# Kernel optimization log

Measured on AMD Instinct MI355X. Metric: run time of the kernel, lower is better.

Reference implementation:

```python
import jax, jax.numpy as jnp
import numpy as np

N_SRC = 50000
N_DST = 50000
N_EDGES = 500000
HIDDEN = 128
HEADS = 8
HEAD_DIM = HIDDEN // HEADS
SCALE = HEAD_DIM ** -0.5


def setup_inputs() -> dict:
    key = jax.random.key(0)
    ks = jax.random.split(key, 12)
    lim = 1.0 / np.sqrt(HIDDEN)
    def lin(k):
        kw, kb = jax.random.split(k)
        W = jax.random.uniform(kw, (HIDDEN, HIDDEN), jnp.float32, -lim, lim)
        b = jax.random.uniform(kb, (HIDDEN,), jnp.float32, -lim, lim)
        return W, b
    Wq, bq = lin(ks[0]); Wk, bk = lin(ks[1]); Wv, bv = lin(ks[2]); Wo, bo = lin(ks[3])
    return {
        "x_src": jax.random.normal(ks[4], (N_SRC, HIDDEN), jnp.float32),
        "x_dst": jax.random.normal(ks[5], (N_DST, HIDDEN), jnp.float32),
        "edge_index": jax.random.randint(ks[6], (2, N_EDGES), 0, N_SRC, jnp.int64),
        "Wq": Wq, "bq": bq, "Wk": Wk, "bk": bk, "Wv": Wv, "bv": bv,
        "Wo": Wo, "bo": bo,
        "edge_bias": jax.random.normal(ks[7], (HEADS,), jnp.float32) * 0.02,
    }


def reference(x_src, x_dst, edge_index, Wq, bq, Wk, bk, Wv, bv, Wo, bo, edge_bias):
    num_dst = x_dst.shape[0]
    # projections (torch Linear: y = x W^T + b), reshape to (N, H, D)
    q = (x_dst @ Wq.T + bq).reshape(num_dst, HEADS, HEAD_DIM)
    k = (x_src @ Wk.T + bk).reshape(-1, HEADS, HEAD_DIM)
    v = (x_src @ Wv.T + bv).reshape(-1, HEADS, HEAD_DIM)
    src_idx, dst_idx = edge_index[0], edge_index[1]
    # per-edge dot-product scores: (E, H)
    scores = (q[dst_idx] * k[src_idx]).sum(-1) * SCALE + edge_bias
    # sparse softmax over edges grouped by destination
    m = jax.ops.segment_max(scores, dst_idx, num_segments=num_dst)  # (N_dst, H)
    e = jnp.exp(scores - m[dst_idx])
    s = jax.ops.segment_sum(e, dst_idx, num_segments=num_dst)  # (N_dst, H)
    w = e / (s[dst_idx] + 1e-8)  # (E, H)
    # scatter-add aggregate weighted values
    out = jax.ops.segment_sum(w[:, :, None] * v[src_idx], dst_idx, num_segments=num_dst)
    out = out.reshape(num_dst, HIDDEN)
    return out @ Wo.T + bo
```

## Files before the change

kernel.cpp:

```cpp
#include <hip/hip_runtime.h>
#include <math.h>

#define HIDDEN 128
#define SCALE 0.25f

typedef __attribute__((ext_vector_type(8))) short short8v;
typedef __attribute__((ext_vector_type(4))) float f32x4;

__device__ __forceinline__ unsigned short f2bf(float f) {
  const unsigned u = __float_as_uint(f);
  const unsigned r = u + 0x7fffu + ((u >> 16) & 1u);
  return (unsigned short)(r >> 16);
}
__device__ __forceinline__ float bflo(unsigned u) { return __uint_as_float(u << 16); }
__device__ __forceinline__ float bfhi(unsigned u) { return __uint_as_float(u & 0xffff0000u); }

__global__ __launch_bounds__(256) void prep_kernel(
    const float* __restrict__ W0, const float* __restrict__ W1,
    const float* __restrict__ W2, const float* __restrict__ W3,
    unsigned short* __restrict__ Wfrag,
    const int* __restrict__ ei, int E, int* __restrict__ counts)
{
  if (blockIdx.x < 32) {
    const int chunk = blockIdx.x * 256 + threadIdx.x;
    const int m = chunk >> 11;
    const int rem = chunk & 2047;
    const int l = rem & 63;
    const int nkk = rem >> 6;
    const int n = nkk >> 2, kk = nkk & 3;
    const float* W = (m == 0) ? W0 : (m == 1) ? W1 : (m == 2) ? W2 : W3;
    const int row = n * 16 + (l & 15);
    const int k0 = kk * 32 + (l >> 4) * 8;
    const float4 v0 = *(const float4*)&W[row * 128 + k0];
    const float4 v1 = *(const float4*)&W[row * 128 + k0 + 4];
    uint4 o;
    o.x = (unsigned)f2bf(v0.x) | ((unsigned)f2bf(v0.y) << 16);
    o.y = (unsigned)f2bf(v0.z) | ((unsigned)f2bf(v0.w) << 16);
    o.z = (unsigned)f2bf(v1.x) | ((unsigned)f2bf(v1.y) << 16);
    o.w = (unsigned)f2bf(v1.z) | ((unsigned)f2bf(v1.w) << 16);
    *(uint4*)&Wfrag[(size_t)chunk * 8] = o;
  } else {
    const int e = ((blockIdx.x - 32) * 256 + threadIdx.x) * 4;
    if (e + 4 <= E) {
      const int4 d = *(const int4*)&ei[E + e];
      atomicAdd(&counts[d.x], 1);
      atomicAdd(&counts[d.y], 1);
      atomicAdd(&counts[d.z], 1);
      atomicAdd(&counts[d.w], 1);
    } else {
      for (int k = e; k < E; ++k) atomicAdd(&counts[ei[E + k]], 1);
    }
  }
}

__global__ __launch_bounds__(256) void qkv_gemm_kernel(
    const float* __restrict__ x_src, const float* __restrict__ x_dst,
    const unsigned short* __restrict__ Wfrag,
    const float* __restrict__ bq, const float* __restrict__ bk,
    const float* __restrict__ bv,
    unsigned short* __restrict__ qb, unsigned short* __restrict__ kvb,
    int Nsrc, int Ndst, int gb_src)
{
  __shared__ __align__(16) char XsB[64 * 256];
  const int t = threadIdx.x;
  const bool isQ = (int)blockIdx.x >= gb_src;
  const int blk = isQ ? ((int)blockIdx.x - gb_src) : (int)blockIdx.x;
  const int N = isQ ? Ndst : Nsrc;
  const float* Xf = isQ ? x_dst : x_src;
  const int row_base = blk * 64;

  float4 xv[8];
  #pragma unroll
  for (int it = 0; it < 8; ++it) {
    const int c = t + it * 256;
    const int row = c >> 5, fc = (c & 31) << 2;
    const int g = row_base + row;
    xv[it] = make_float4(0.f, 0.f, 0.f, 0.f);
    if (g < N) xv[it] = *(const float4*)&Xf[(size_t)g * 128 + fc];
  }
  #pragma unroll
  for (int it = 0; it < 8; ++it) {
    const int c = t + it * 256;
    const int row = c >> 5, b8 = (c & 31) << 3;
    uint2 p;
    p.x = (unsigned)f2bf(xv[it].x) | ((unsigned)f2bf(xv[it].y) << 16);
    p.y = (unsigned)f2bf(xv[it].z) | ((unsigned)f2bf(xv[it].w) << 16);
    *(uint2*)&XsB[row * 256 + (b8 ^ ((row & 7) << 4))] = p;
  }
  __syncthreads();

  const int l = t & 63, w = t >> 6;
  const int r16 = l & 15, g16 = l >> 4;
  const int sw = (r16 & 7) << 4;
  const char* ax = &XsB[(w * 16 + r16) * 256];

  if (isQ) {
    f32x4 acc[8];
    #pragma unroll
    for (int n = 0; n < 8; ++n) acc[n] = (f32x4){0.f, 0.f, 0.f, 0.f};
    const short8v* wf = (const short8v*)Wfrag + l;
    #pragma unroll
    for (int kk = 0; kk < 4; ++kk) {
      const short8v a = *(const short8v*)(ax + ((kk * 64 + g16 * 16) ^ sw));
      #pragma unroll
      for (int n = 0; n < 8; ++n)
        acc[n] = __builtin_amdgcn_mfma_f32_16x16x32_bf16(a, wf[(n * 4 + kk) * 64], acc[n], 0, 0, 0);
    }
    #pragma unroll
    for (int n = 0; n < 8; ++n) {
      const int col = n * 16 + r16;
      const float bvv = bq[col];
      #pragma unroll
      for (int r = 0; r < 4; ++r) {
        const int g = row_base + w * 16 + g16 * 4 + r;
        if (g < N) qb[(size_t)g * 128 + col] = f2bf(acc[n][r] + bvv);
      }
    }
  } else {
    f32x4 accK[8], accV[8];
    #pragma unroll
    for (int n = 0; n < 8; ++n) {
      accK[n] = (f32x4){0.f, 0.f, 0.f, 0.f};
      accV[n] = (f32x4){0.f, 0.f, 0.f, 0.f};
    }
    const short8v* wfk = (const short8v*)(Wfrag + 16384) + l;
    const short8v* wfv = (const short8v*)(Wfrag + 32768) + l;
    #pragma unroll
    for (int kk = 0; kk < 4; ++kk) {
      const short8v a = *(const short8v*)(ax + ((kk * 64 + g16 * 16) ^ sw));
      #pragma unroll
      for (int n = 0; n < 8; ++n) {
        accK[n] = __builtin_amdgcn_mfma_f32_16x16x32_bf16(a, wfk[(n * 4 + kk) * 64], accK[n], 0, 0, 0);
        accV[n] = __builtin_amdgcn_mfma_f32_16x16x32_bf16(a, wfv[(n * 4 + kk) * 64], accV[n], 0, 0, 0);
      }
    }
    #pragma unroll
    for (int n = 0; n < 8; ++n) {
      const int col = n * 16 + r16;
      const float bkk = bk[col], bvv = bv[col];
      #pragma unroll
      for (int r = 0; r < 4; ++r) {
        const int g = row_base + w * 16 + g16 * 4 + r;
        if (g < N) {
          kvb[(size_t)g * 256 + col]       = f2bf(accK[n][r] + bkk);
          kvb[(size_t)g * 256 + 128 + col] = f2bf(accV[n][r] + bvv);
        }
      }
    }
  }
}

__global__ __launch_bounds__(256) void out_gemm_kernel(
    const unsigned short* __restrict__ Xh,
    const unsigned short* __restrict__ Wfrag_o,
    const float* __restrict__ bo, float* __restrict__ Y, int N)
{
  __shared__ __align__(16) char XsB[64 * 256];
  const int t = threadIdx.x;
  const int row_base = blockIdx.x * 64;

  uint2 hv[8];
  #pragma unroll
  for (int it = 0; it < 8; ++it) {
    const int c = t + it * 256;
    const int row = c >> 5, fc = (c & 31) << 2;
    const int g = row_base + row;
    hv[it] = make_uint2(0, 0);
    if (g < N) hv[it] = *(const uint2*)&Xh[(size_t)g * 128 + fc];
  }
  #pragma unroll
  for (int it = 0; it < 8; ++it) {
    const int c = t + it * 256;
    const int row = c >> 5, b8 = (c & 31) << 3;
    *(uint2*)&XsB[row * 256 + (b8 ^ ((row & 7) << 4))] = hv[it];
  }
  __syncthreads();

  const int l = t & 63, w = t >> 6;
  const int r16 = l & 15, g16 = l >> 4;
  const int sw = (r16 & 7) << 4;
  f32x4 acc[8];
  #pragma unroll
  for (int n = 0; n < 8; ++n) acc[n] = (f32x4){0.f, 0.f, 0.f, 0.f};
  const char* ax = &XsB[(w * 16 + r16) * 256];
  const short8v* wf = (const short8v*)Wfrag_o + l;
  #pragma unroll
  for (int kk = 0; kk < 4; ++kk) {
    const short8v a = *(const short8v*)(ax + ((kk * 64 + g16 * 16) ^ sw));
    #pragma unroll
    for (int n = 0; n < 8; ++n)
      acc[n] = __builtin_amdgcn_mfma_f32_16x16x32_bf16(a, wf[(n * 4 + kk) * 64], acc[n], 0, 0, 0);
  }
  #pragma unroll
  for (int n = 0; n < 8; ++n) {
    const int col = n * 16 + r16;
    const float bvv = bo[col];
    #pragma unroll
    for (int r = 0; r < 4; ++r) {
      const int g = row_base + w * 16 + g16 * 4 + r;
      if (g < N) Y[(size_t)g * 128 + col] = acc[n][r] + bvv;
    }
  }
}

__global__ __launch_bounds__(256) void reduce_counts_kernel(
    const int* __restrict__ counts, int n, int* __restrict__ bsums)
{
  const int idx = blockIdx.x * 256 + threadIdx.x;
  int x = (idx < n) ? counts[idx] : 0;
  #pragma unroll
  for (int off = 1; off < 64; off <<= 1) x += __shfl_xor(x, off);
  __shared__ int ws[4];
  if ((threadIdx.x & 63) == 0) ws[threadIdx.x >> 6] = x;
  __syncthreads();
  if (threadIdx.x == 0) bsums[blockIdx.x] = ws[0] + ws[1] + ws[2] + ws[3];
}

__global__ __launch_bounds__(256) void scan_bsums_kernel(int* bsums, int nb)
{
  __shared__ int buf[256];
  const int t = threadIdx.x;
  const int x = (t < nb) ? bsums[t] : 0;
  buf[t] = x;
  __syncthreads();
  int val = x;
  #pragma unroll
  for (int off = 1; off < 256; off <<= 1) {
    const int other = (t >= off) ? buf[t - off] : 0;
    __syncthreads();
    val += other;
    buf[t] = val;
    __syncthreads();
  }
  if (t < nb) bsums[t] = val - x;
}

__global__ __launch_bounds__(256) void scan_counts_kernel(
    const int* __restrict__ counts, int n, const int* __restrict__ bsums,
    int* __restrict__ offsets)
{
  const int idx = blockIdx.x * 256 + threadIdx.x;
  const int lane = threadIdx.x & 63, wid = threadIdx.x >> 6;
  const int x = (idx < n) ? counts[idx] : 0;
  int v = x;
  #pragma unroll
  for (int off = 1; off < 64; off <<= 1) {
    const int t2 = __shfl_up(v, off);
    if (lane >= off) v += t2;
  }
  __shared__ int wsum[4];
  if (lane == 63) wsum[wid] = v;
  __syncthreads();
  int wbase = 0;
  for (int p = 0; p < wid; ++p) wbase += wsum[p];
  if (idx < n) offsets[idx] = bsums[blockIdx.x] + wbase + v - x;
}

__global__ __launch_bounds__(256) void scatter_kernel(
    const int* __restrict__ ei, int E, const int* __restrict__ offsets,
    int* __restrict__ cursor, int* __restrict__ csr_src)
{
  const int e = (blockIdx.x * 256 + threadIdx.x) * 4;
  if (e + 4 <= E) {
    const int4 s = *(const int4*)&ei[e];
    const int4 d = *(const int4*)&ei[E + e];
    int p;
    p = atomicAdd(&cursor[d.x], 1); csr_src[offsets[d.x] + p] = s.x;
    p = atomicAdd(&cursor[d.y], 1); csr_src[offsets[d.y] + p] = s.y;
    p = atomicAdd(&cursor[d.z], 1); csr_src[offsets[d.z] + p] = s.z;
    p = atomicAdd(&cursor[d.w], 1); csr_src[offsets[d.w] + p] = s.w;
  } else {
    for (int k = e; k < E; ++k) {
      const int d = ei[E + k];
      const int p = atomicAdd(&cursor[d], 1);
      csr_src[offsets[d] + p] = ei[k];
    }
  }
}

__global__ __launch_bounds__(256) void edge_attn_kernel(
    const unsigned short* __restrict__ qb, const unsigned short* __restrict__ kvb,
    const float* __restrict__ eb, const int* __restrict__ offsets,
    const int* __restrict__ counts, const int* __restrict__ csr_src,
    unsigned short* __restrict__ agg, int Ndst)
{
  const int wave = blockIdx.x * 4 + (threadIdx.x >> 6);
  if (wave >= Ndst) return;
  const int lane = threadIdx.x & 63;
  const int eg = lane >> 3, h = lane & 7;

  const uint4 q0 = *(const uint4*)&qb[(size_t)wave * 128 + h * 16];
  const uint4 q1 = *(const uint4*)&qb[(size_t)wave * 128 + h * 16 + 8];
  const float bias = eb[h];
  const int ro = offsets[wave];
  const int cnt = counts[wave];

  float acc[16];
  #pragma unroll
  for (int j = 0; j < 16; ++j) acc[j] = 0.f;
  float s = 0.f;

  for (int it = 0; it * 8 < cnt; ++it) {
    const int e = it * 8 + eg;
    const bool act = e < cnt;
    const int src = act ? csr_src[ro + e] : 0;
    const size_t base = (size_t)src * 256 + h * 16;
    const uint4 k0 = *(const uint4*)&kvb[base];
    const uint4 k1 = *(const uint4*)&kvb[base + 8];
    const uint4 v0 = *(const uint4*)&kvb[base + 128];
    const uint4 v1 = *(const uint4*)&kvb[base + 136];

    float p = 0.f;
    p = fmaf(bflo(q0.x), bflo(k0.x), p); p = fmaf(bfhi(q0.x), bfhi(k0.x), p);
    p = fmaf(bflo(q0.y), bflo(k0.y), p); p = fmaf(bfhi(q0.y), bfhi(k0.y), p);
    p = fmaf(bflo(q0.z), bflo(k0.z), p); p = fmaf(bfhi(q0.z), bfhi(k0.z), p);
    p = fmaf(bflo(q0.w), bflo(k0.w), p); p = fmaf(bfhi(q0.w), bfhi(k0.w), p);
    p = fmaf(bflo(q1.x), bflo(k1.x), p); p = fmaf(bfhi(q1.x), bfhi(k1.x), p);
    p = fmaf(bflo(q1.y), bflo(k1.y), p); p = fmaf(bfhi(q1.y), bfhi(k1.y), p);
    p = fmaf(bflo(q1.z), bflo(k1.z), p); p = fmaf(bfhi(q1.z), bfhi(k1.z), p);
    p = fmaf(bflo(q1.w), bflo(k1.w), p); p = fmaf(bfhi(q1.w), bfhi(k1.w), p);

    const float wgt = act ? __expf(fmaf(p, SCALE, bias)) : 0.f;
    s += wgt;
    acc[0]  = fmaf(wgt, bflo(v0.x), acc[0]);  acc[1]  = fmaf(wgt, bfhi(v0.x), acc[1]);
    acc[2]  = fmaf(wgt, bflo(v0.y), acc[2]);  acc[3]  = fmaf(wgt, bfhi(v0.y), acc[3]);
    acc[4]  = fmaf(wgt, bflo(v0.z), acc[4]);  acc[5]  = fmaf(wgt, bfhi(v0.z), acc[5]);
    acc[6]  = fmaf(wgt, bflo(v0.w), acc[6]);  acc[7]  = fmaf(wgt, bfhi(v0.w), acc[7]);
    acc[8]  = fmaf(wgt, bflo(v1.x), acc[8]);  acc[9]  = fmaf(wgt, bfhi(v1.x), acc[9]);
    acc[10] = fmaf(wgt, bflo(v1.y), acc[10]); acc[11] = fmaf(wgt, bfhi(v1.y), acc[11]);
    acc[12] = fmaf(wgt, bflo(v1.z), acc[12]); acc[13] = fmaf(wgt, bfhi(v1.z), acc[13]);
    acc[14] = fmaf(wgt, bflo(v1.w), acc[14]); acc[15] = fmaf(wgt, bfhi(v1.w), acc[15]);
  }

  #pragma unroll
  for (int m = 8; m <= 32; m <<= 1) {
    s += __shfl_xor(s, m);
    #pragma unroll
    for (int j = 0; j < 16; ++j) acc[j] += __shfl_xor(acc[j], m);
  }

  if (eg == 0) {
    const float rs = 1.0f / (s + 1e-8f);
    uint4 o0, o1;
    o0.x = (unsigned)f2bf(acc[0] * rs)  | ((unsigned)f2bf(acc[1] * rs) << 16);
    o0.y = (unsigned)f2bf(acc[2] * rs)  | ((unsigned)f2bf(acc[3] * rs) << 16);
    o0.z = (unsigned)f2bf(acc[4] * rs)  | ((unsigned)f2bf(acc[5] * rs) << 16);
    o0.w = (unsigned)f2bf(acc[6] * rs)  | ((unsigned)f2bf(acc[7] * rs) << 16);
    o1.x = (unsigned)f2bf(acc[8] * rs)  | ((unsigned)f2bf(acc[9] * rs) << 16);
    o1.y = (unsigned)f2bf(acc[10] * rs) | ((unsigned)f2bf(acc[11] * rs) << 16);
    o1.z = (unsigned)f2bf(acc[12] * rs) | ((unsigned)f2bf(acc[13] * rs) << 16);
    o1.w = (unsigned)f2bf(acc[14] * rs) | ((unsigned)f2bf(acc[15] * rs) << 16);
    *(uint4*)&agg[(size_t)wave * 128 + h * 16] = o0;
    *(uint4*)&agg[(size_t)wave * 128 + h * 16 + 8] = o1;
  }
}

extern "C" void kernel_launch(void* const* d_in, const int* in_sizes, int n_in,
                              void* d_out, int out_size, void* d_ws, size_t ws_size,
                              hipStream_t stream) {
  const float* x_src = (const float*)d_in[0];
  const float* x_dst = (const float*)d_in[1];
  const int*   ei    = (const int*)d_in[2];
  const float* Wq = (const float*)d_in[3];
  const float* bq = (const float*)d_in[4];
  const float* Wk = (const float*)d_in[5];
  const float* bk = (const float*)d_in[6];
  const float* Wv = (const float*)d_in[7];
  const float* bv = (const float*)d_in[8];
  const float* Wo = (const float*)d_in[9];
  const float* bo = (const float*)d_in[10];
  const float* eb = (const float*)d_in[11];

  const int Nsrc = in_sizes[0] / HIDDEN;
  const int Ndst = in_sizes[1] / HIDDEN;
  const int E    = in_sizes[2] / 2;

  char* w = (char*)d_ws;
  unsigned short* qb   = (unsigned short*)w; w += (size_t)Ndst * 128 * 2;
  unsigned short* kvb  = (unsigned short*)w; w += (size_t)Nsrc * 256 * 2;
  unsigned short* aggb = (unsigned short*)w; w += (size_t)Ndst * 128 * 2;
  unsigned short* Wb   = (unsigned short*)w; w += (size_t)4 * 16384 * 2;
  int* counts  = (int*)w; w += (size_t)Ndst * sizeof(int);
  int* cursor  = (int*)w; w += (size_t)Ndst * sizeof(int);
  int* offsets = (int*)w; w += (size_t)Ndst * sizeof(int);
  int* bsums   = (int*)w; w += 256 * sizeof(int);
  int* csr_src = (int*)w; w += (size_t)E * sizeof(int);

  hipMemsetAsync(counts, 0, (size_t)Ndst * 2 * sizeof(int), stream);

  dim3 blk256(256);
  const int e4blocks = (E / 4 + 255) / 256;
  prep_kernel<<<32 + e4blocks, blk256, 0, stream>>>(Wq, Wk, Wv, Wo, Wb, ei, E, counts);

  const int gb_dst = (Ndst + 63) / 64;
  const int gb_src = (Nsrc + 63) / 64;
  qkv_gemm_kernel<<<gb_src + gb_dst, blk256, 0, stream>>>(
      x_src, x_dst, Wb, bq, bk, bv, qb, kvb, Nsrc, Ndst, gb_src);

  const int nb = (Ndst + 255) / 256;
  reduce_counts_kernel<<<nb, blk256, 0, stream>>>(counts, Ndst, bsums);
  scan_bsums_kernel<<<1, blk256, 0, stream>>>(bsums, nb);
  scan_counts_kernel<<<nb, blk256, 0, stream>>>(counts, Ndst, bsums, offsets);

  scatter_kernel<<<e4blocks, blk256, 0, stream>>>(ei, E, offsets, cursor, csr_src);

  const int ablocks = (Ndst + 3) / 4;
  edge_attn_kernel<<<ablocks, blk256, 0, stream>>>(qb, kvb, eb, offsets, counts,
                                                   csr_src, aggb, Ndst);

  out_gemm_kernel<<<gb_dst, blk256, 0, stream>>>(aggb, Wb + 49152, bo, (float*)d_out, Ndst);
}
```

Baseline: 172.9 us.

## Make projection GEMMs persistent with register-resident weights and double-buffered tiles

The QKV and output GEMMs become persistent kernels with a fixed grid. Each block loads its weight fragments into registers once, then loops over row tiles, prefetching the next tile into a second LDS buffer while computing the current one. QKV is split per projection type, and the output GEMM loads tiles with direct global-to-LDS loads. Bias is folded into the accumulator init, MFMA operands are swapped for row-contiguous vector stores, and bf16 packing uses the hardware pack instruction. This trades higher register pressure and fewer blocks for reduced redundant weight loads and hidden load latency. No barriers guard the LDS buffers between waves, but each wave only touches its own 16 rows, so this appears safe.

```diff
diff --git a/kernel.cpp b/kernel.cpp
--- a/kernel.cpp
+++ b/kernel.cpp
@@ -3,6 +3,8 @@
 
 #define HIDDEN 128
 #define SCALE 0.25f
+#define NB_TYPE 170
+#define NB_O 256
 
 typedef __attribute__((ext_vector_type(8))) short short8v;
 typedef __attribute__((ext_vector_type(4))) float f32x4;
@@ -12,8 +14,19 @@
   const unsigned r = u + 0x7fffu + ((u >> 16) & 1u);
   return (unsigned short)(r >> 16);
 }
+__device__ __forceinline__ unsigned pack_bf2(float a, float b) {
+  unsigned r;
+  asm("v_cvt_pk_bf16_f32 %0, %1, %2" : "=v"(r) : "v"(a), "v"(b));
+  return r;
+}
 __device__ __forceinline__ float bflo(unsigned u) { return __uint_as_float(u << 16); }
 __device__ __forceinline__ float bfhi(unsigned u) { return __uint_as_float(u & 0xffff0000u); }
+
+__device__ __forceinline__ void gload_lds16(const void* g, void* l) {
+  __builtin_amdgcn_global_load_lds(
+      (const __attribute__((address_space(1))) unsigned*)g,
+      (__attribute__((address_space(3))) unsigned*)l, 16, 0, 0);
+}
 
 __global__ __launch_bounds__(256) void prep_kernel(
     const float* __restrict__ W0, const float* __restrict__ W1,
@@ -53,153 +66,166 @@
   }
 }
 
-__global__ __launch_bounds__(256) void qkv_gemm_kernel(
+__global__ __launch_bounds__(256, 2) void qkv_gemm_kernel(
     const float* __restrict__ x_src, const float* __restrict__ x_dst,
     const unsigned short* __restrict__ Wfrag,
     const float* __restrict__ bq, const float* __restrict__ bk,
     const float* __restrict__ bv,
     unsigned short* __restrict__ qb, unsigned short* __restrict__ kvb,
-    int Nsrc, int Ndst, int gb_src)
-{
-  __shared__ __align__(16) char XsB[64 * 256];
+    int Nsrc, int Ndst)
+{
+  __shared__ __align__(16) char Xs[2][16384];
   const int t = threadIdx.x;
-  const bool isQ = (int)blockIdx.x >= gb_src;
-  const int blk = isQ ? ((int)blockIdx.x - gb_src) : (int)blockIdx.x;
-  const int N = isQ ? Ndst : Nsrc;
-  const float* Xf = isQ ? x_dst : x_src;
-  const int row_base = blk * 64;
-
-  float4 xv[8];
-  #pragma unroll
-  for (int it = 0; it < 8; ++it) {
-    const int c = t + it * 256;
-    const int row = c >> 5, fc = (c & 31) << 2;
-    const int g = row_base + row;
-    xv[it] = make_float4(0.f, 0.f, 0.f, 0.f);
-    if (g < N) xv[it] = *(const float4*)&Xf[(size_t)g * 128 + fc];
-  }
-  #pragma unroll
-  for (int it = 0; it < 8; ++it) {
-    const int c = t + it * 256;
-    const int row = c >> 5, b8 = (c & 31) << 3;
-    uint2 p;
-    p.x = (unsigned)f2bf(xv[it].x) | ((unsigned)f2bf(xv[it].y) << 16);
-    p.y = (unsigned)f2bf(xv[it].z) | ((unsigned)f2bf(xv[it].w) << 16);
-    *(uint2*)&XsB[row * 256 + (b8 ^ ((row & 7) << 4))] = p;
-  }
-  __syncthreads();
-
   const int l = t & 63, w = t >> 6;
   const int r16 = l & 15, g16 = l >> 4;
-  const int sw = (r16 & 7) << 4;
-  const char* ax = &XsB[(w * 16 + r16) * 256];
-
-  if (isQ) {
+
+  int bid = blockIdx.x;
+  const float* X; const float* bias; const unsigned short* wbase;
+  unsigned short* out; int ostride, ooff, N;
+  if (bid < NB_TYPE)          { X = x_src; bias = bk; wbase = Wfrag + 16384; out = kvb; ostride = 256; ooff = 0;   N = Nsrc; }
+  else if (bid < 2 * NB_TYPE) { bid -= NB_TYPE;   X = x_src; bias = bv; wbase = Wfrag + 32768; out = kvb; ostride = 256; ooff = 128; N = Nsrc; }
+  else                        { bid -= 2 * NB_TYPE; X = x_dst; bias = bq; wbase = Wfrag;       out = qb;  ostride = 128; ooff = 0;   N = Ndst; }
+  const int ntiles = (N + 63) >> 6;
+
+  short8v wfr[32];
+  #pragma unroll
+  for (int i = 0; i < 32; ++i) wfr[i] = ((const short8v*)wbase)[i * 64 + l];
+
+  const int srow = l >> 5;
+  const int scol = (l & 31) * 4;
+
+  float4 xv[8];
+  int tile = bid;
+  {
+    #pragma unroll
+    for (int j = 0; j < 8; ++j) {
+      const int r = j * 2 + srow;
+      const int g = tile * 64 + w * 16 + r;
+      xv[j] = make_float4(0.f, 0.f, 0.f, 0.f);
+      if (g < N) xv[j] = *(const float4*)&X[(size_t)g * 128 + scol];
+    }
+    #pragma unroll
+    for (int j = 0; j < 8; ++j) {
+      const int r = j * 2 + srow;
+      uint2 p;
+      p.x = pack_bf2(xv[j].x, xv[j].y);
+      p.y = pack_bf2(xv[j].z, xv[j].w);
+      *(uint2*)&Xs[0][(w * 16 + r) * 256 + ((scol * 2) ^ ((r & 7) << 4))] = p;
+    }
+  }
+  int cur = 0;
+  for (; tile < ntiles; tile += NB_TYPE) {
+    const int nt = tile + NB_TYPE;
+    if (nt < ntiles) {
+      #pragma unroll
+      for (int j = 0; j < 8; ++j) {
+        const int r = j * 2 + srow;
+        const int g = nt * 64 + w * 16 + r;
+        xv[j] = make_float4(0.f, 0.f, 0.f, 0.f);
+        if (g < N) xv[j] = *(const float4*)&X[(size_t)g * 128 + scol];
+      }
+    }
     f32x4 acc[8];
     #pragma unroll
-    for (int n = 0; n < 8; ++n) acc[n] = (f32x4){0.f, 0.f, 0.f, 0.f};
-    const short8v* wf = (const short8v*)Wfrag + l;
+    for (int n = 0; n < 8; ++n) {
+      const float4 bb = *(const float4*)&bias[n * 16 + g16 * 4];
+      acc[n] = (f32x4){bb.x, bb.y, bb.z, bb.w};
+    }
+    const char* ax = &Xs[cur][(w * 16 + r16) * 256];
     #pragma unroll
     for (int kk = 0; kk < 4; ++kk) {
-      const short8v a = *(const short8v*)(ax + ((kk * 64 + g16 * 16) ^ sw));
+      const short8v b = *(const short8v*)(ax + ((kk * 64 + g16 * 16) ^ ((r16 & 7) << 4)));
       #pragma unroll
       for (int n = 0; n < 8; ++n)
-        acc[n] = __builtin_amdgcn_mfma_f32_16x16x32_bf16(a, wf[(n * 4 + kk) * 64], acc[n], 0, 0, 0);
-    }
-    #pragma unroll
-    for (int n = 0; n < 8; ++n) {
-      const int col = n * 16 + r16;
-      const float bvv = bq[col];
-      #pragma unroll
-      for (int r = 0; r < 4; ++r) {
-        const int g = row_base + w * 16 + g16 * 4 + r;
-        if (g < N) qb[(size_t)g * 128 + col] = f2bf(acc[n][r] + bvv);
+        acc[n] = __builtin_amdgcn_mfma_f32_16x16x32_bf16(wfr[n * 4 + kk], b, acc[n], 0, 0, 0);
+    }
+    const int grow = tile * 64 + w * 16 + r16;
+    if (grow < N) {
+      unsigned short* orow = out + (size_t)grow * ostride + ooff;
+      #pragma unroll
+      for (int n = 0; n < 8; ++n) {
+        uint2 o;
+        o.x = pack_bf2(acc[n][0], acc[n][1]);
+        o.y = pack_bf2(acc[n][2], acc[n][3]);
+        *(uint2*)&orow[n * 16 + g16 * 4] = o;
       }
     }
-  } else {
-    f32x4 accK[8], accV[8];
-    #pragma unroll
-    for (int n = 0; n < 8; ++n) {
-      accK[n] = (f32x4){0.f, 0.f, 0.f, 0.f};
-      accV[n] = (f32x4){0.f, 0.f, 0.f, 0.f};
-    }
-    const short8v* wfk = (const short8v*)(Wfrag + 16384) + l;
-    const short8v* wfv = (const short8v*)(Wfrag + 32768) + l;
-    #pragma unroll
-    for (int kk = 0; kk < 4; ++kk) {
-      const short8v a = *(const short8v*)(ax + ((kk * 64 + g16 * 16) ^ sw));
-      #pragma unroll
-      for (int n = 0; n < 8; ++n) {
-        accK[n] = __builtin_amdgcn_mfma_f32_16x16x32_bf16(a, wfk[(n * 4 + kk) * 64], accK[n], 0, 0, 0);
-        accV[n] = __builtin_amdgcn_mfma_f32_16x16x32_bf16(a, wfv[(n * 4 + kk) * 64], accV[n], 0, 0, 0);
+    if (nt < ntiles) {
+      #pragma unroll
+      for (int j = 0; j < 8; ++j) {
+        const int r = j * 2 + srow;
+        uint2 p;
+        p.x = pack_bf2(xv[j].x, xv[j].y);
+        p.y = pack_bf2(xv[j].z, xv[j].w);
+        *(uint2*)&Xs[cur ^ 1][(w * 16 + r) * 256 + ((scol * 2) ^ ((r & 7) << 4))] = p;
       }
     }
-    #pragma unroll
-    for (int n = 0; n < 8; ++n) {
-      const int col = n * 16 + r16;
-      const float bkk = bk[col], bvv = bv[col];
-      #pragma unroll
-      for (int r = 0; r < 4; ++r) {
-        const int g = row_base + w * 16 + g16 * 4 + r;
-        if (g < N) {
-          kvb[(size_t)g * 256 + col]       = f2bf(accK[n][r] + bkk);
-          kvb[(size_t)g * 256 + 128 + col] = f2bf(accV[n][r] + bvv);
-        }
-      }
-    }
-  }
-}
-
-__global__ __launch_bounds__(256) void out_gemm_kernel(
-    const unsigned short* __restrict__ Xh,
-    const unsigned short* __restrict__ Wfrag_o,
+    cur ^= 1;
+  }
+}
+
+__global__ __launch_bounds__(256, 2) void out_gemm_kernel(
+    const unsigned short* __restrict__ agg, const unsigned short* __restrict__ Wo_frag,
     const float* __restrict__ bo, float* __restrict__ Y, int N)
 {
-  __shared__ __align__(16) char XsB[64 * 256];
+  __shared__ __align__(16) char Xs[2][16384];
   const int t = threadIdx.x;
-  const int row_base = blockIdx.x * 64;
-
-  uint2 hv[8];
-  #pragma unroll
-  for (int it = 0; it < 8; ++it) {
-    const int c = t + it * 256;
-    const int row = c >> 5, fc = (c & 31) << 2;
-    const int g = row_base + row;
-    hv[it] = make_uint2(0, 0);
-    if (g < N) hv[it] = *(const uint2*)&Xh[(size_t)g * 128 + fc];
-  }
-  #pragma unroll
-  for (int it = 0; it < 8; ++it) {
-    const int c = t + it * 256;
-    const int row = c >> 5, b8 = (c & 31) << 3;
-    *(uint2*)&XsB[row * 256 + (b8 ^ ((row & 7) << 4))] = hv[it];
-  }
-  __syncthreads();
-
   const int l = t & 63, w = t >> 6;
   const int r16 = l & 15, g16 = l >> 4;
-  const int sw = (r16 & 7) << 4;
-  f32x4 acc[8];
-  #pragma unroll
-  for (int n = 0; n < 8; ++n) acc[n] = (f32x4){0.f, 0.f, 0.f, 0.f};
-  const char* ax = &XsB[(w * 16 + r16) * 256];
-  const short8v* wf = (const short8v*)Wfrag_o + l;
-  #pragma unroll
-  for (int kk = 0; kk < 4; ++kk) {
-    const short8v a = *(const short8v*)(ax + ((kk * 64 + g16 * 16) ^ sw));
-    #pragma unroll
-    for (int n = 0; n < 8; ++n)
-      acc[n] = __builtin_amdgcn_mfma_f32_16x16x32_bf16(a, wf[(n * 4 + kk) * 64], acc[n], 0, 0, 0);
-  }
-  #pragma unroll
-  for (int n = 0; n < 8; ++n) {
-    const int col = n * 16 + r16;
-    const float bvv = bo[col];
-    #pragma unroll
-    for (int r = 0; r < 4; ++r) {
-      const int g = row_base + w * 16 + g16 * 4 + r;
-      if (g < N) Y[(size_t)g * 128 + col] = acc[n][r] + bvv;
-    }
+  const int ntiles = (N + 63) >> 6;
+
+  short8v wfr[32];
+  #pragma unroll
+  for (int i = 0; i < 32; ++i) wfr[i] = ((const short8v*)Wo_frag)[i * 64 + l];
+
+  int tile = blockIdx.x;
+  {
+    #pragma unroll
+    for (int it = 0; it < 4; ++it) {
+      const int row16 = it * 4 + (l >> 4);
+      const int grow = tile * 64 + w * 16 + row16;
+      const int sb = ((l & 15) * 16) ^ ((row16 & 7) << 4);
+      gload_lds16((const char*)agg + (size_t)grow * 256 + sb,
+                  &Xs[0][w * 4096 + it * 1024 + l * 16]);
+    }
+  }
+  int cur = 0;
+  for (; tile < ntiles; tile += NB_O) {
+    const int nt = tile + NB_O;
+    asm volatile("s_waitcnt vmcnt(0)" ::: "memory");
+    __builtin_amdgcn_sched_barrier(0);
+    if (nt < ntiles) {
+      #pragma unroll
+      for (int it = 0; it < 4; ++it) {
+        const int row16 = it * 4 + (l >> 4);
+        const int grow = nt * 64 + w * 16 + row16;
+        const int sb = ((l & 15) * 16) ^ ((row16 & 7) << 4);
+        gload_lds16((const char*)agg + (size_t)grow * 256 + sb,
+                    &Xs[cur ^ 1][w * 4096 + it * 1024 + l * 16]);
+      }
+    }
+    f32x4 acc[8];
+    #pragma unroll
+    for (int n = 0; n < 8; ++n) {
+      const float4 bb = *(const float4*)&bo[n * 16 + g16 * 4];
+      acc[n] = (f32x4){bb.x, bb.y, bb.z, bb.w};
+    }
+    const char* ax = &Xs[cur][(w * 16 + r16) * 256];
+    #pragma unroll
+    for (int kk = 0; kk < 4; ++kk) {
+      const short8v b = *(const short8v*)(ax + ((kk * 64 + g16 * 16) ^ ((r16 & 7) << 4)));
+      #pragma unroll
+      for (int n = 0; n < 8; ++n)
+        acc[n] = __builtin_amdgcn_mfma_f32_16x16x32_bf16(wfr[n * 4 + kk], b, acc[n], 0, 0, 0);
+    }
+    const int grow = tile * 64 + w * 16 + r16;
+    if (grow < N) {
+      float* yrow = Y + (size_t)grow * 128;
+      #pragma unroll
+      for (int n = 0; n < 8; ++n)
+        *(float4*)&yrow[n * 16 + g16 * 4] = make_float4(acc[n][0], acc[n][1], acc[n][2], acc[n][3]);
+    }
+    cur ^= 1;
   }
 }
 
@@ -342,14 +368,14 @@
   if (eg == 0) {
     const float rs = 1.0f / (s + 1e-8f);
     uint4 o0, o1;
-    o0.x = (unsigned)f2bf(acc[0] * rs)  | ((unsigned)f2bf(acc[1] * rs) << 16);
-    o0.y = (unsigned)f2bf(acc[2] * rs)  | ((unsigned)f2bf(acc[3] * rs) << 16);
-    o0.z = (unsigned)f2bf(acc[4] * rs)  | ((unsigned)f2bf(acc[5] * rs) << 16);
-    o0.w = (unsigned)f2bf(acc[6] * rs)  | ((unsigned)f2bf(acc[7] * rs) << 16);
-    o1.x = (unsigned)f2bf(acc[8] * rs)  | ((unsigned)f2bf(acc[9] * rs) << 16);
-    o1.y = (unsigned)f2bf(acc[10] * rs) | ((unsigned)f2bf(acc[11] * rs) << 16);
-    o1.z = (unsigned)f2bf(acc[12] * rs) | ((unsigned)f2bf(acc[13] * rs) << 16);
-    o1.w = (unsigned)f2bf(acc[14] * rs) | ((unsigned)f2bf(acc[15] * rs) << 16);
+    o0.x = pack_bf2(acc[0] * rs,  acc[1] * rs);
+    o0.y = pack_bf2(acc[2] * rs,  acc[3] * rs);
+    o0.z = pack_bf2(acc[4] * rs,  acc[5] * rs);
+    o0.w = pack_bf2(acc[6] * rs,  acc[7] * rs);
+    o1.x = pack_bf2(acc[8] * rs,  acc[9] * rs);
+    o1.y = pack_bf2(acc[10] * rs, acc[11] * rs);
+    o1.z = pack_bf2(acc[12] * rs, acc[13] * rs);
+    o1.w = pack_bf2(acc[14] * rs, acc[15] * rs);
     *(uint4*)&agg[(size_t)wave * 128 + h * 16] = o0;
     *(uint4*)&agg[(size_t)wave * 128 + h * 16 + 8] = o1;
   }
@@ -392,10 +418,8 @@
   const int e4blocks = (E / 4 + 255) / 256;
   prep_kernel<<<32 + e4blocks, blk256, 0, stream>>>(Wq, Wk, Wv, Wo, Wb, ei, E, counts);
 
-  const int gb_dst = (Ndst + 63) / 64;
-  const int gb_src = (Nsrc + 63) / 64;
-  qkv_gemm_kernel<<<gb_src + gb_dst, blk256, 0, stream>>>(
-      x_src, x_dst, Wb, bq, bk, bv, qb, kvb, Nsrc, Ndst, gb_src);
+  qkv_gemm_kernel<<<3 * NB_TYPE, blk256, 0, stream>>>(
+      x_src, x_dst, Wb, bq, bk, bv, qb, kvb, Nsrc, Ndst);
 
   const int nb = (Ndst + 255) / 256;
   reduce_counts_kernel<<<nb, blk256, 0, stream>>>(counts, Ndst, bsums);
@@ -408,5 +432,5 @@
   edge_attn_kernel<<<ablocks, blk256, 0, stream>>>(qb, kvb, eb, offsets, counts,
                                                    csr_src, aggb, Ndst);
 
-  out_gemm_kernel<<<gb_dst, blk256, 0, stream>>>(aggb, Wb + 49152, bo, (float*)d_out, Ndst);
-}
+  out_gemm_kernel<<<NB_O, blk256, 0, stream>>>(aggb, Wb + 49152, bo, (float*)d_out, Ndst);
+}
```

Result: faster. 146.0 us (-15.6%).
